# Kernel tuning notes

Hardware: AMD Instinct MI355X
Metric: run time of the kernel (lower is better)

The kernel has to match this reference:

```python
import jax, jax.numpy as jnp
import numpy as np

IN_DIM = 1024
OUT_DIM = 65536
BATCH = 32
MASK_DENSITY = 0.1  # fraction of weights kept, mimicking LSH neuron selection


def setup_inputs() -> dict:
    key = jax.random.key(0)
    kx, kw, km = jax.random.split(key, 3)
    x = jax.random.normal(kx, (BATCH, IN_DIM), dtype=jnp.float32)
    w = jax.random.normal(kw, (IN_DIM, OUT_DIM), dtype=jnp.float32) * 0.05
    mask = (jax.random.uniform(km, (IN_DIM, OUT_DIM)) < MASK_DENSITY).astype(jnp.float32)
    b = jnp.zeros((OUT_DIM,), dtype=jnp.float32)
    return {"x": x, "mask": mask, "w": w, "b": b}


def reference(x, mask, w, b):
    # Faithful math of: sparse_dense_matmul(x, from_dense(w * squeeze(mask))) + b
    # which is exactly x @ (w * mask) + b in dense form.
    masked_w = w * mask  # [in, out]
    return jnp.matmul(x, masked_w) + b  # [batch, out]
```

## Files before the change

### kernel.cpp

```cpp
#include <hip/hip_runtime.h>


#define IN_DIM 1024
#define OUT_DIM 65536
#define BATCH 32
#define KSPLIT 4
#define KCHUNK (IN_DIM / KSPLIT)
#define BLOCK 256
#define U 8
#define NG (KCHUNK / U)
#define XT_FLOATS (IN_DIM * BATCH)

__global__ __launch_bounds__(BLOCK) void sl_transpose(
    const float* __restrict__ x, float* __restrict__ xT) {
  int idx = blockIdx.x * BLOCK + threadIdx.x;
  int i = idx >> 10;
  int k = idx & (IN_DIM - 1);
  xT[k * BATCH + i] = x[idx];
}

template <bool ATOMIC, bool TRANSPOSED>
__global__ __launch_bounds__(BLOCK, 4) void sl_main(
    const float* __restrict__ xbase, const float* __restrict__ mask,
    const float* __restrict__ w, float* __restrict__ dst) {
  const int tid = threadIdx.x;
  const int j = blockIdx.x * BLOCK + tid;
  const int kc = blockIdx.y;
  const int k0 = kc * KCHUNK;

  float acc[BATCH];
#pragma unroll
  for (int i = 0; i < BATCH; ++i) acc[i] = 0.0f;

  const float* wp = w + (size_t)k0 * OUT_DIM + j;
  const float* mp = mask + (size_t)k0 * OUT_DIM + j;

  float wA[U], mA[U], wB[U], mB[U];

  auto loadg = [&](int g, float* wv, float* mv) {
#pragma unroll
    for (int u = 0; u < U; ++u) {
      size_t off = (size_t)(g * U + u) * OUT_DIM;
      wv[u] = __builtin_nontemporal_load(wp + off);
      mv[u] = __builtin_nontemporal_load(mp + off);
    }
  };
  auto computeg = [&](int g, const float* wv, const float* mv) {
#pragma unroll
    for (int u = 0; u < U; ++u) {
      float wm = wv[u] * mv[u];
      if (TRANSPOSED) {
        const float4* xk =
            (const float4*)(xbase + (size_t)(k0 + g * U + u) * BATCH);
#pragma unroll
        for (int q = 0; q < BATCH / 4; ++q) {
          float4 xq = xk[q];
          acc[q * 4 + 0] = fmaf(xq.x, wm, acc[q * 4 + 0]);
          acc[q * 4 + 1] = fmaf(xq.y, wm, acc[q * 4 + 1]);
          acc[q * 4 + 2] = fmaf(xq.z, wm, acc[q * 4 + 2]);
          acc[q * 4 + 3] = fmaf(xq.w, wm, acc[q * 4 + 3]);
        }
      } else {
        int k = k0 + g * U + u;
#pragma unroll
        for (int i = 0; i < BATCH; ++i)
          acc[i] = fmaf(xbase[(size_t)i * IN_DIM + k], wm, acc[i]);
      }
    }
  };

  loadg(0, wA, mA);
#pragma unroll 1
  for (int g = 0; g < NG; g += 2) {
    loadg(g + 1, wB, mB);
    computeg(g, wA, mA);
    if (g + 2 < NG) loadg(g + 2, wA, mA);
    computeg(g + 1, wB, mB);
  }

  if (ATOMIC) {
#pragma unroll
    for (int i = 0; i < BATCH; ++i)
      atomicAdd(dst + (size_t)i * OUT_DIM + j, acc[i]);
  } else {
#pragma unroll
    for (int i = 0; i < BATCH; ++i)
      __builtin_nontemporal_store(
          acc[i], dst + (size_t)(kc * BATCH + i) * OUT_DIM + j);
  }
}

__global__ __launch_bounds__(BLOCK) void sl_reduce(
    const float* __restrict__ part, const float* __restrict__ b,
    float* __restrict__ out) {
  const int j4 = blockIdx.x * BLOCK + threadIdx.x;
  const int i = blockIdx.y;
  float4 s = ((const float4*)b)[j4];
#pragma unroll
  for (int kc = 0; kc < KSPLIT; ++kc) {
    float4 p =
        ((const float4*)part)[(size_t)(kc * BATCH + i) * (OUT_DIM / 4) + j4];
    s.x += p.x; s.y += p.y; s.z += p.z; s.w += p.w;
  }
  ((float4*)out)[(size_t)i * (OUT_DIM / 4) + j4] = s;
}

__global__ __launch_bounds__(BLOCK) void sl_init(
    const float* __restrict__ b, float* __restrict__ out) {
  const int j4 = blockIdx.x * BLOCK + threadIdx.x;
  const float4 bv = ((const float4*)b)[j4];
#pragma unroll
  for (int i = 0; i < BATCH; ++i)
    ((float4*)out)[(size_t)i * (OUT_DIM / 4) + j4] = bv;
}

extern "C" void kernel_launch(void* const* d_in, const int* in_sizes, int n_in,
                              void* d_out, int out_size, void* d_ws, size_t ws_size,
                              hipStream_t stream) {
  const float* x = (const float*)d_in[0];
  const float* mask = (const float*)d_in[1];
  const float* w = (const float*)d_in[2];
  const float* b = (const float*)d_in[3];
  float* out = (float*)d_out;

  const size_t xt_bytes = XT_FLOATS * sizeof(float);
  const size_t part_bytes =
      (size_t)KSPLIT * BATCH * OUT_DIM * sizeof(float);
  float* xT = (float*)d_ws;
  float* part = (float*)d_ws + XT_FLOATS;

  if (ws_size >= xt_bytes + part_bytes) {
    hipLaunchKernelGGL(sl_transpose, dim3(XT_FLOATS / BLOCK), dim3(BLOCK), 0,
                       stream, x, xT);
    hipLaunchKernelGGL((sl_main<false, true>), dim3(OUT_DIM / BLOCK, KSPLIT),
                       dim3(BLOCK), 0, stream, xT, mask, w, part);
    hipLaunchKernelGGL(sl_reduce, dim3(OUT_DIM / 4 / BLOCK, BATCH), dim3(BLOCK),
                       0, stream, part, b, out);
  } else if (ws_size >= xt_bytes) {
    hipLaunchKernelGGL(sl_init, dim3(OUT_DIM / 4 / BLOCK), dim3(BLOCK), 0,
                       stream, b, out);
    hipLaunchKernelGGL(sl_transpose, dim3(XT_FLOATS / BLOCK), dim3(BLOCK), 0,
                       stream, x, xT);
    hipLaunchKernelGGL((sl_main<true, true>), dim3(OUT_DIM / BLOCK, KSPLIT),
                       dim3(BLOCK), 0, stream, xT, mask, w, out);
  } else {
    hipLaunchKernelGGL(sl_init, dim3(OUT_DIM / 4 / BLOCK), dim3(BLOCK), 0,
                       stream, b, out);
    hipLaunchKernelGGL((sl_main<true, false>), dim3(OUT_DIM / BLOCK, KSPLIT),
                       dim3(BLOCK), 0, stream, x, mask, w, out);
  }
}
```

Measured before the change: 610.3 us.

## Compute masked matmul with bf16 MFMA instead of scalar FP32 FMAs

Replaces the per-thread scalar FMA inner product with 32x32x16 bf16 MFMA instructions. A prep kernel packs x into bf16 A-fragments, and w*mask is converted to bf16 per lane as the B fragment. KSPLIT drops from 4 to 2, and the partial-sum layout follows the MFMA output row mapping. The kernel is bound by streaming w and mask (512 MB), so the aim is to cut ALU and issue overhead so the loads dominate, at the cost of bf16 precision loss on both operands.

```diff
diff --git a/kernel.cpp b/kernel.cpp
--- a/kernel.cpp
+++ b/kernel.cpp
@@ -1,92 +1,108 @@
 #include <hip/hip_runtime.h>
+#include <hip/hip_bf16.h>
 
 
 #define IN_DIM 1024
 #define OUT_DIM 65536
 #define BATCH 32
-#define KSPLIT 4
-#define KCHUNK (IN_DIM / KSPLIT)
 #define BLOCK 256
-#define U 8
-#define NG (KCHUNK / U)
-#define XT_FLOATS (IN_DIM * BATCH)
+#define JT 32
+#define BJT 128
+#define KSPLIT 2
+#define NSTEP_TOT (IN_DIM / 16)
+#define NSTEP (NSTEP_TOT / KSPLIT)
+#define XA_USHORTS (NSTEP_TOT * 64 * 8)
 
-__global__ __launch_bounds__(BLOCK) void sl_transpose(
-    const float* __restrict__ x, float* __restrict__ xT) {
-  int idx = blockIdx.x * BLOCK + threadIdx.x;
-  int i = idx >> 10;
-  int k = idx & (IN_DIM - 1);
-  xT[k * BATCH + i] = x[idx];
+typedef short bf16x8 __attribute__((ext_vector_type(8)));
+typedef float f32x16 __attribute__((ext_vector_type(16)));
+
+__device__ __forceinline__ short f2bf(float f) {
+  __hip_bfloat16 h = __float2bfloat16(f);
+  return __builtin_bit_cast(short, h);
 }
 
-template <bool ATOMIC, bool TRANSPOSED>
-__global__ __launch_bounds__(BLOCK, 4) void sl_main(
-    const float* __restrict__ xbase, const float* __restrict__ mask,
+__global__ __launch_bounds__(BLOCK) void sl_prepA(
+    const float* __restrict__ x, ushort* __restrict__ xA) {
+  int idx = blockIdx.x * BLOCK + threadIdx.x;
+  int t = idx >> 6;
+  int l = idx & 63;
+  int m = l & 31;
+  int kk = t * 16 + (l >> 5) * 8;
+  const float* xp = x + m * IN_DIM + kk;
+  bf16x8 a;
+#pragma unroll
+  for (int j = 0; j < 8; ++j) a[j] = f2bf(xp[j]);
+  *(bf16x8*)(xA + (size_t)idx * 8) = a;
+}
+
+template <bool ATOMIC, bool PREPPED>
+__global__ __launch_bounds__(BLOCK, 4) void sl_mfma(
+    const void* __restrict__ xsrc, const float* __restrict__ mask,
     const float* __restrict__ w, float* __restrict__ dst) {
   const int tid = threadIdx.x;
-  const int j = blockIdx.x * BLOCK + tid;
+  const int lane = tid & 63;
+  const int wid = tid >> 6;
+  const int jb = blockIdx.x * BJT + wid * JT;
   const int kc = blockIdx.y;
-  const int k0 = kc * KCHUNK;
+  const int t0 = kc * NSTEP;
+  const int col = lane & 31;
+  const int kh = lane >> 5;
 
-  float acc[BATCH];
+  const size_t jcol = (size_t)jb + col;
+  const float* wp = w + (size_t)(t0 * 16 + kh * 8) * OUT_DIM + jcol;
+  const float* mp = mask + (size_t)(t0 * 16 + kh * 8) * OUT_DIM + jcol;
+
+  f32x16 acc;
 #pragma unroll
-  for (int i = 0; i < BATCH; ++i) acc[i] = 0.0f;
+  for (int i = 0; i < 16; ++i) acc[i] = 0.0f;
 
-  const float* wp = w + (size_t)k0 * OUT_DIM + j;
-  const float* mp = mask + (size_t)k0 * OUT_DIM + j;
+  float wbuf[2][8], mbuf[2][8];
+  bf16x8 abuf[2];
 
-  float wA[U], mA[U], wB[U], mB[U];
-
-  auto loadg = [&](int g, float* wv, float* mv) {
+  auto loadg = [&](int s, int p) {
+    const size_t base = (size_t)s * 16 * OUT_DIM;
 #pragma unroll
-    for (int u = 0; u < U; ++u) {
-      size_t off = (size_t)(g * U + u) * OUT_DIM;
-      wv[u] = __builtin_nontemporal_load(wp + off);
-      mv[u] = __builtin_nontemporal_load(mp + off);
+    for (int u = 0; u < 8; ++u) {
+      wbuf[p][u] = __builtin_nontemporal_load(wp + base + (size_t)u * OUT_DIM);
+      mbuf[p][u] = __builtin_nontemporal_load(mp + base + (size_t)u * OUT_DIM);
     }
-  };
-  auto computeg = [&](int g, const float* wv, const float* mv) {
+    if (PREPPED) {
+      const ushort* xA = (const ushort*)xsrc;
+      abuf[p] = *(const bf16x8*)(xA + ((size_t)(t0 + s) * 64 + lane) * 8);
+    } else {
+      const float* x = (const float*)xsrc;
+      const float* xp = x + col * IN_DIM + (t0 + s) * 16 + kh * 8;
+      bf16x8 a;
 #pragma unroll
-    for (int u = 0; u < U; ++u) {
-      float wm = wv[u] * mv[u];
-      if (TRANSPOSED) {
-        const float4* xk =
-            (const float4*)(xbase + (size_t)(k0 + g * U + u) * BATCH);
-#pragma unroll
-        for (int q = 0; q < BATCH / 4; ++q) {
-          float4 xq = xk[q];
-          acc[q * 4 + 0] = fmaf(xq.x, wm, acc[q * 4 + 0]);
-          acc[q * 4 + 1] = fmaf(xq.y, wm, acc[q * 4 + 1]);
-          acc[q * 4 + 2] = fmaf(xq.z, wm, acc[q * 4 + 2]);
-          acc[q * 4 + 3] = fmaf(xq.w, wm, acc[q * 4 + 3]);
-        }
-      } else {
-        int k = k0 + g * U + u;
-#pragma unroll
-        for (int i = 0; i < BATCH; ++i)
-          acc[i] = fmaf(xbase[(size_t)i * IN_DIM + k], wm, acc[i]);
-      }
+      for (int j = 0; j < 8; ++j) a[j] = f2bf(xp[j]);
+      abuf[p] = a;
     }
   };
 
-  loadg(0, wA, mA);
+  auto computeg = [&](int p) {
+    bf16x8 bfrag;
+#pragma unroll
+    for (int u = 0; u < 8; ++u) bfrag[u] = f2bf(wbuf[p][u] * mbuf[p][u]);
+    acc = __builtin_amdgcn_mfma_f32_32x32x16_bf16(abuf[p], bfrag, acc, 0, 0, 0);
+  };
+
+  loadg(0, 0);
 #pragma unroll 1
-  for (int g = 0; g < NG; g += 2) {
-    loadg(g + 1, wB, mB);
-    computeg(g, wA, mA);
-    if (g + 2 < NG) loadg(g + 2, wA, mA);
-    computeg(g + 1, wB, mB);
+  for (int s = 0; s < NSTEP - 1; ++s) {
+    loadg(s + 1, (s + 1) & 1);
+    computeg(s & 1);
   }
+  computeg((NSTEP - 1) & 1);
 
-  if (ATOMIC) {
 #pragma unroll
-    for (int i = 0; i < BATCH; ++i)
-      atomicAdd(dst + (size_t)i * OUT_DIM + j, acc[i]);
-  } else {
-#pragma unroll
-    for (int i = 0; i < BATCH; ++i)
+  for (int r = 0; r < 16; ++r) {
+    int row = (r & 3) + 8 * (r >> 2) + 4 * kh;
+    if (ATOMIC) {
+      atomicAdd(dst + (size_t)row * OUT_DIM + jcol, acc[r]);
+    } else {
       __builtin_nontemporal_store(
-          acc[i], dst + (size_t)(kc * BATCH + i) * OUT_DIM + j);
+          acc[r], dst + (size_t)(kc * BATCH + row) * OUT_DIM + jcol);
+    }
   }
 }
 
@@ -123,30 +139,30 @@
   const float* b = (const float*)d_in[3];
   float* out = (float*)d_out;
 
-  const size_t xt_bytes = XT_FLOATS * sizeof(float);
+  const size_t xa_bytes = (size_t)XA_USHORTS * sizeof(ushort);
   const size_t part_bytes =
       (size_t)KSPLIT * BATCH * OUT_DIM * sizeof(float);
-  float* xT = (float*)d_ws;
-  float* part = (float*)d_ws + XT_FLOATS;
+  ushort* xA = (ushort*)d_ws;
+  float* part = (float*)((char*)d_ws + xa_bytes);
 
-  if (ws_size >= xt_bytes + part_bytes) {
-    hipLaunchKernelGGL(sl_transpose, dim3(XT_FLOATS / BLOCK), dim3(BLOCK), 0,
-                       stream, x, xT);
-    hipLaunchKernelGGL((sl_main<false, true>), dim3(OUT_DIM / BLOCK, KSPLIT),
-                       dim3(BLOCK), 0, stream, xT, mask, w, part);
+  if (ws_size >= xa_bytes + part_bytes) {
+    hipLaunchKernelGGL(sl_prepA, dim3(XA_USHORTS / 8 / BLOCK), dim3(BLOCK), 0,
+                       stream, x, xA);
+    hipLaunchKernelGGL((sl_mfma<false, true>), dim3(OUT_DIM / BJT, KSPLIT),
+                       dim3(BLOCK), 0, stream, xA, mask, w, part);
     hipLaunchKernelGGL(sl_reduce, dim3(OUT_DIM / 4 / BLOCK, BATCH), dim3(BLOCK),
                        0, stream, part, b, out);
-  } else if (ws_size >= xt_bytes) {
+  } else if (ws_size >= xa_bytes) {
     hipLaunchKernelGGL(sl_init, dim3(OUT_DIM / 4 / BLOCK), dim3(BLOCK), 0,
                        stream, b, out);
-    hipLaunchKernelGGL(sl_transpose, dim3(XT_FLOATS / BLOCK), dim3(BLOCK), 0,
-                       stream, x, xT);
-    hipLaunchKernelGGL((sl_main<true, true>), dim3(OUT_DIM / BLOCK, KSPLIT),
-                       dim3(BLOCK), 0, stream, xT, mask, w, out);
+    hipLaunchKernelGGL(sl_prepA, dim3(XA_USHORTS / 8 / BLOCK), dim3(BLOCK), 0,
+                       stream, x, xA);
+    hipLaunchKernelGGL((sl_mfma<true, true>), dim3(OUT_DIM / BJT, KSPLIT),
+                       dim3(BLOCK), 0, stream, xA, mask, w, out);
   } else {
     hipLaunchKernelGGL(sl_init, dim3(OUT_DIM / 4 / BLOCK), dim3(BLOCK), 0,
                        stream, b, out);
-    hipLaunchKernelGGL((sl_main<true, false>), dim3(OUT_DIM / BLOCK, KSPLIT),
+    hipLaunchKernelGGL((sl_mfma<true, false>), dim3(OUT_DIM / BJT, KSPLIT),
                        dim3(BLOCK), 0, stream, x, mask, w, out);
   }
 }
```

After: 575.5 us. 5.7% less time.
